# Kernel tuning notes

Hardware: AMD Instinct MI355X
Metric: run time of the kernel (lower is better)

Reference implementation:

```python
import jax, jax.numpy as jnp
import numpy as np

T, B, E, H = 128, 1024, 1024, 1024  # batch must equal hidden (original code uses Whh @ h)


def setup_inputs() -> dict:
    key = jax.random.key(0)
    ks = jax.random.split(key, 10)
    s = 1.0 / np.sqrt(H).astype(np.float32)  # ~xavier scale, avoids gate saturation
    inp = {
        'X': jax.random.normal(ks[0], (T, B, E), dtype=jnp.float32),
        'Wii': jax.random.normal(ks[1], (E, H), dtype=jnp.float32) * s,
        'Whi': jax.random.normal(ks[2], (H, H), dtype=jnp.float32) * s,
        'bi': jnp.zeros((H,), dtype=jnp.float32),
        'Wif': jax.random.normal(ks[3], (E, H), dtype=jnp.float32) * s,
        'Whf': jax.random.normal(ks[4], (H, H), dtype=jnp.float32) * s,
        'bf': jnp.zeros((H,), dtype=jnp.float32),
        'Wig': jax.random.normal(ks[5], (E, H), dtype=jnp.float32) * s,
        'Whg': jax.random.normal(ks[6], (H, H), dtype=jnp.float32) * s,
        'bg': jnp.zeros((H,), dtype=jnp.float32),
        'Wio': jax.random.normal(ks[7], (E, H), dtype=jnp.float32) * s,
        'Who': jax.random.normal(ks[8], (H, H), dtype=jnp.float32) * s,
        'bo': jnp.zeros((H,), dtype=jnp.float32),
    }
    return inp


def reference(X, Wii, Whi, bi, Wif, Whf, bf, Wig, Whg, bg, Wio, Who, bo):
    # Faithful to the original: recurrent term is Whh @ h (NOT h @ Whh),
    # which requires batch == hidden as in the source module.
    batch = X.shape[1]
    hid = Wii.shape[1]
    h0 = jnp.zeros((batch, hid), dtype=X.dtype)
    c0 = jnp.zeros((batch, hid), dtype=X.dtype)

    def step(carry, x_t):
        h, c = carry
        i = jax.nn.sigmoid(x_t @ Wii + Whi @ h + bi)
        f = jax.nn.sigmoid(x_t @ Wif + Whf @ h + bf)
        g = jnp.tanh(x_t @ Wig + Whg @ h + bg)
        o = jax.nn.sigmoid(x_t @ Wio + Who @ h + bo)
        c_new = f * c + i * g
        h_new = o * jnp.tanh(c_new)
        return (h_new, c_new), h_new

    (h_t, c_t), hidden_sequence = jax.lax.scan(step, (h0, c0), X)
    return hidden_sequence, (h_t, c_t)
```

## Files before the change

### kernel.cpp

```cpp
#include <hip/hip_runtime.h>
#include <cstdint>

typedef __attribute__((ext_vector_type(8))) short bf16x8;
typedef __attribute__((ext_vector_type(4))) float f32x4;
typedef __attribute__((ext_vector_type(4))) unsigned int u32x4;

#define AS1 __attribute__((address_space(1)))
#define AS3 __attribute__((address_space(3)))

__device__ __forceinline__ unsigned short f2bf(float f) {
  unsigned int u = __builtin_bit_cast(unsigned int, f);
  return (unsigned short)((u + 0x7fffu + ((u >> 16) & 1u)) >> 16);
}
__device__ __forceinline__ float bf2f(unsigned short h) {
  unsigned int u = ((unsigned int)h) << 16;
  return __builtin_bit_cast(float, u);
}
__device__ __forceinline__ float sigm(float x) { return 1.f / (1.f + __expf(-x)); }
__device__ __forceinline__ float tanh_f(float x) {
  float e = __expf(2.f * x);
  return 1.f - 2.f / (e + 1.f);
}
__device__ __forceinline__ void gload16(const void* g, void* l) {
  __builtin_amdgcn_global_load_lds((const AS1 unsigned int*)g, (AS3 unsigned int*)l, 16, 0, 0);
}
__device__ __forceinline__ int swz(int e) { return e ^ (((e >> 6) & 7) << 3); }


__global__ __launch_bounds__(256) void conv_wh_kernel(
    const float4* __restrict__ w0, const float4* __restrict__ w1,
    const float4* __restrict__ w2, const float4* __restrict__ w3,
    unsigned long long* __restrict__ dst) {
  int i = blockIdx.x * 256 + threadIdx.x;
  int g = i >> 18;
  const float4* s = g == 0 ? w0 : g == 1 ? w1 : g == 2 ? w2 : w3;
  float4 v = s[i & 0x3FFFF];
  unsigned long long p = (unsigned long long)f2bf(v.x) |
                         ((unsigned long long)f2bf(v.y) << 16) |
                         ((unsigned long long)f2bf(v.z) << 32) |
                         ((unsigned long long)f2bf(v.w) << 48);
  dst[i] = p;
}

__global__ __launch_bounds__(256) void conv_wiT_kernel(
    const float* __restrict__ w0, const float* __restrict__ w1,
    const float* __restrict__ w2, const float* __restrict__ w3,
    unsigned short* __restrict__ dst) {
  __shared__ unsigned short ls[64][72];
  int bid = blockIdx.x;
  int g = bid >> 8;
  int t2 = bid & 255;
  int tj = t2 & 15, tk = t2 >> 4;
  const float* W = g == 0 ? w0 : g == 1 ? w1 : g == 2 ? w2 : w3;
  int k0 = tk * 64, j0 = tj * 64;
  int ty = threadIdx.x >> 6, tx = threadIdx.x & 63;
#pragma unroll
  for (int r = 0; r < 16; ++r) {
    int k = k0 + ty * 16 + r;
    ls[tx][ty * 16 + r] = f2bf(W[k * 1024 + j0 + tx]);
  }
  __syncthreads();
#pragma unroll
  for (int r = 0; r < 16; ++r) {
    int jl = ty * 16 + r;
    dst[(size_t)(g * 1024 + j0 + jl) * 1024 + k0 + tx] = ls[jl][tx];
  }
}

__global__ __launch_bounds__(256) void conv_bias_kernel(
    const float* __restrict__ b0, const float* __restrict__ b1,
    const float* __restrict__ b2, const float* __restrict__ b3,
    float* __restrict__ dst) {
  int i = blockIdx.x * 256 + threadIdx.x;
  const float* s = (i >> 10) == 0 ? b0 : (i >> 10) == 1 ? b1 : (i >> 10) == 2 ? b2 : b3;
  dst[i] = s[i & 1023];
}

__global__ __launch_bounds__(256) void conv_x_kernel(
    const float4* __restrict__ src, unsigned long long* __restrict__ dst, int n4) {
  int i = blockIdx.x * 256 + threadIdx.x;
  if (i < n4) {
    float4 v = src[i];
    dst[i] = (unsigned long long)f2bf(v.x) |
             ((unsigned long long)f2bf(v.y) << 16) |
             ((unsigned long long)f2bf(v.z) << 32) |
             ((unsigned long long)f2bf(v.w) << 48);
  }
}

__global__ __launch_bounds__(512) void xproj_gemm_kernel(
    const unsigned short* __restrict__ A,
    const unsigned short* __restrict__ Bt,
    unsigned short* __restrict__ C,
    int Mc) {
  __shared__ __align__(16) unsigned short smem[2][2][256 * 64];
  int xcd = blockIdx.x & 7;
  int i5 = blockIdx.x >> 3;
  int bn = xcd * 2 + (i5 & 1);
  int bm = i5 >> 1;
  int m0 = bm * 256, n0 = bn * 256;
  int tid = threadIdx.x, w = tid >> 6, lane = tid & 63;
  int wm = w >> 2, wn = w & 3;
  int l15 = lane & 15, l4 = lane >> 4;

  f32x4 acc[8][4];
#pragma unroll
  for (int i = 0; i < 8; ++i)
#pragma unroll
    for (int j = 0; j < 4; ++j) acc[i][j] = (f32x4)0.f;

  auto stageHalf = [&](int buf, int kt, int X) {
    int kk = kt * 64;
    unsigned short* dst = &smem[buf][X & 1][0];
    const unsigned short* src = (X & 1) ? Bt : A;
    int gbase = (X & 1) ? n0 : m0;
    int r0 = (X >> 1) * 128;
#pragma unroll
    for (int u = 0; u < 2; ++u) {
      int cid = u * 512 + tid;
      int rl = r0 + (cid >> 3), s = cid & 7;
      int sk = kk + ((s ^ (rl & 7)) << 3);
      gload16(&src[(size_t)(gbase + rl) * 1024 + sk],
              &dst[r0 * 64 + (u * 512 + w * 64) * 8]);
    }
  };
  auto rdA = [&](int buf, int lo, bf16x8 (&arr)[4][2]) {
#pragma unroll
    for (int mf = 0; mf < 4; ++mf)
#pragma unroll
      for (int kss = 0; kss < 2; ++kss) {
        int row = lo * 128 + wm * 64 + mf * 16 + l15;
        arr[mf][kss] =
            *(const bf16x8*)&smem[buf][0][swz(row * 64 + kss * 32 + l4 * 8)];
      }
  };
  auto rdB = [&](int buf, int lo, bf16x8 (&arr)[2][2]) {
#pragma unroll
    for (int nf = 0; nf < 2; ++nf)
#pragma unroll
      for (int kss = 0; kss < 2; ++kss) {
        int row = lo * 128 + wn * 32 + nf * 16 + l15;
        arr[nf][kss] =
            *(const bf16x8*)&smem[buf][1][swz(row * 64 + kss * 32 + l4 * 8)];
      }
  };

  bf16x8 af03[4][2], af47[4][2], bfr01[2][2], bfr23[2][2];

  stageHalf(0, 0, 0); stageHalf(0, 0, 1); stageHalf(0, 0, 2); stageHalf(0, 0, 3);

  for (int t = 0; t < 16; ++t) {
    int c = t & 1;
    if (t < 15) asm volatile("s_waitcnt vmcnt(6)" ::: "memory");
    else        asm volatile("s_waitcnt vmcnt(6)" ::: "memory");
    __builtin_amdgcn_sched_barrier(0);
    __builtin_amdgcn_s_barrier();
    __builtin_amdgcn_sched_barrier(0);
    rdA(c, 0, af03);
    if (t + 1 < 16) stageHalf(c ^ 1, t + 1, 0);
    asm volatile("s_waitcnt lgkmcnt(0)" ::: "memory");
    __builtin_amdgcn_sched_barrier(0);
    if (t > 0) {
      __builtin_amdgcn_s_setprio(1);
#pragma unroll
      for (int mf = 0; mf < 4; ++mf)
#pragma unroll
        for (int nf = 0; nf < 2; ++nf)
#pragma unroll
          for (int kss = 0; kss < 2; ++kss)
            acc[4 + mf][2 + nf] = __builtin_amdgcn_mfma_f32_16x16x32_bf16(
                af47[mf][kss], bfr23[nf][kss], acc[4 + mf][2 + nf], 0, 0, 0);
      __builtin_amdgcn_s_setprio(0);
    }
    if (t < 15) asm volatile("s_waitcnt vmcnt(6)" ::: "memory");
    else        asm volatile("s_waitcnt vmcnt(4)" ::: "memory");
    __builtin_amdgcn_sched_barrier(0);
    __builtin_amdgcn_s_barrier();
    __builtin_amdgcn_sched_barrier(0);
    rdB(c, 0, bfr01);
    if (t + 1 < 16) stageHalf(c ^ 1, t + 1, 1);
    asm volatile("s_waitcnt lgkmcnt(0)" ::: "memory");
    __builtin_amdgcn_sched_barrier(0);
    __builtin_amdgcn_s_setprio(1);
#pragma unroll
    for (int mf = 0; mf < 4; ++mf)
#pragma unroll
      for (int nf = 0; nf < 2; ++nf)
#pragma unroll
        for (int kss = 0; kss < 2; ++kss)
          acc[mf][nf] = __builtin_amdgcn_mfma_f32_16x16x32_bf16(
              af03[mf][kss], bfr01[nf][kss], acc[mf][nf], 0, 0, 0);
    __builtin_amdgcn_s_setprio(0);
    if (t < 15) asm volatile("s_waitcnt vmcnt(6)" ::: "memory");
    else        asm volatile("s_waitcnt vmcnt(2)" ::: "memory");
    __builtin_amdgcn_sched_barrier(0);
    __builtin_amdgcn_s_barrier();
    __builtin_amdgcn_sched_barrier(0);
    rdA(c, 1, af47);
    if (t + 1 < 16) stageHalf(c ^ 1, t + 1, 2);
    asm volatile("s_waitcnt lgkmcnt(0)" ::: "memory");
    __builtin_amdgcn_sched_barrier(0);
    __builtin_amdgcn_s_setprio(1);
#pragma unroll
    for (int mf = 0; mf < 4; ++mf)
#pragma unroll
      for (int nf = 0; nf < 2; ++nf)
#pragma unroll
        for (int kss = 0; kss < 2; ++kss)
          acc[4 + mf][nf] = __builtin_amdgcn_mfma_f32_16x16x32_bf16(
              af47[mf][kss], bfr01[nf][kss], acc[4 + mf][nf], 0, 0, 0);
    __builtin_amdgcn_s_setprio(0);
    if (t < 15) asm volatile("s_waitcnt vmcnt(6)" ::: "memory");
    else        asm volatile("s_waitcnt vmcnt(0)" ::: "memory");
    __builtin_amdgcn_sched_barrier(0);
    __builtin_amdgcn_s_barrier();
    __builtin_amdgcn_sched_barrier(0);
    rdB(c, 1, bfr23);
    if (t + 1 < 16) stageHalf(c ^ 1, t + 1, 3);
    asm volatile("s_waitcnt lgkmcnt(0)" ::: "memory");
    __builtin_amdgcn_sched_barrier(0);
    __builtin_amdgcn_s_setprio(1);
#pragma unroll
    for (int mf = 0; mf < 4; ++mf)
#pragma unroll
      for (int nf = 0; nf < 2; ++nf)
#pragma unroll
        for (int kss = 0; kss < 2; ++kss)
          acc[mf][2 + nf] = __builtin_amdgcn_mfma_f32_16x16x32_bf16(
              af03[mf][kss], bfr23[nf][kss], acc[mf][2 + nf], 0, 0, 0);
    __builtin_amdgcn_s_setprio(0);
  }
  {
    __builtin_amdgcn_s_setprio(1);
#pragma unroll
    for (int mf = 0; mf < 4; ++mf)
#pragma unroll
      for (int nf = 0; nf < 2; ++nf)
#pragma unroll
        for (int kss = 0; kss < 2; ++kss)
          acc[4 + mf][2 + nf] = __builtin_amdgcn_mfma_f32_16x16x32_bf16(
              af47[mf][kss], bfr23[nf][kss], acc[4 + mf][2 + nf], 0, 0, 0);
    __builtin_amdgcn_s_setprio(0);
  }

  unsigned short* lsC = &smem[0][0][0];
#pragma unroll
  for (int h = 0; h < 2; ++h) {
    __syncthreads();
#pragma unroll
    for (int mf = 0; mf < 8; ++mf)
#pragma unroll
      for (int f = 0; f < 2; ++f) {
        int nf = h * 2 + f;
        int rowl = (mf < 4 ? wm * 64 + mf * 16 : 128 + wm * 64 + (mf - 4) * 16)
                   + l4 * 4;
        int coll = wn * 32 + f * 16 + l15;
#pragma unroll
        for (int r = 0; r < 4; ++r)
          lsC[(rowl + r) * 136 + coll] = f2bf(acc[mf][nf][r]);
      }
    __syncthreads();
#pragma unroll
    for (int u = 0; u < 8; ++u) {
      int chunk = u * 512 + tid;
      int row = chunk >> 4, c8 = chunk & 15;
      u32x4 v = *(const u32x4*)&lsC[row * 136 + c8 * 8];
      __builtin_nontemporal_store(
          v, (u32x4*)&C[(size_t)(m0 + row) * 4096 + n0 + h * 128 + c8 * 8]);
    }
  }
}

__global__ __launch_bounds__(256) void lstm_step_kernel(
    const unsigned short* __restrict__ Wh,
    const unsigned short* __restrict__ hT,
    const unsigned short* __restrict__ Xp,
    const float* __restrict__ bias,
    float* __restrict__ cst,
    float* __restrict__ out_h,
    float* __restrict__ out_ht,
    float* __restrict__ out_ct,
    unsigned short* __restrict__ hT_next,
    int isLast) {
  __shared__ unsigned short lsA[3][128 * 64];
  __shared__ unsigned short lsB[3][64 * 64];
  int bx = blockIdx.x;
  int xcd = bx & 7, idx = bx >> 3;
  int bb = xcd * 4 + (idx & 3);
  int bj = idx >> 2;
  int b0 = bb * 32, j0 = bj * 64;
  int tid = threadIdx.x, w = tid >> 6, lane = tid & 63;
  int wm = w >> 1, wn = w & 1;
  int l15 = lane & 15, l4 = lane >> 4;
  int bbase = b0 + wm * 16 + l4 * 4;

  float bias_pre[4][2];
  float c_pre[2][4];
  unsigned short xp_pre[4][2][4];
#pragma unroll
  for (int n = 0; n < 2; ++n) {
    int j = j0 + wn * 32 + n * 16 + l15;
#pragma unroll
    for (int g = 0; g < 4; ++g) bias_pre[g][n] = bias[g * 1024 + j];
#pragma unroll
    for (int r = 0; r < 4; ++r) {
      c_pre[n][r] = cst[(size_t)(bbase + r) * 1024 + j];
#pragma unroll
      for (int g = 0; g < 4; ++g)
        xp_pre[g][n][r] = Xp[(size_t)(bbase + r) * 4096 + g * 1024 + j];
    }
  }

  f32x4 acc[4][2];
#pragma unroll
  for (int g = 0; g < 4; ++g)
#pragma unroll
    for (int n = 0; n < 2; ++n) acc[g][n] = (f32x4)0.f;

  auto stage = [&](int buf, int kk) {
#pragma unroll
    for (int ld = 0; ld < 4; ++ld) {
      int cid = ld * 256 + tid;
      int r = cid >> 3, kc = (cid & 7) * 8;
      int sk = kk + (kc ^ ((r & 7) << 3));
      int grow = ((r >> 4) & 3) * 1024 + b0 + (r >> 6) * 16 + (r & 15);
      gload16(&Wh[(size_t)grow * 1024 + sk], &lsA[buf][(ld * 256 + w * 64) * 8]);
    }
#pragma unroll
    for (int u = 0; u < 2; ++u) {
      int cid = u * 256 + tid;
      int r = cid >> 3, kc = (cid & 7) * 8;
      int sk = kk + (kc ^ ((r & 7) << 3));
      gload16(&hT[(size_t)(j0 + r) * 1024 + sk], &lsB[buf][(u * 256 + w * 64) * 8]);
    }
  };
  auto compute = [&](int buf) {
    bf16x8 af[4][2], bfr[2][2];
#pragma unroll
    for (int g = 0; g < 4; ++g)
#pragma unroll
      for (int kss = 0; kss < 2; ++kss) {
        int e = (wm * 64 + g * 16 + l15) * 64 + kss * 32 + l4 * 8;
        af[g][kss] = *(const bf16x8*)&lsA[buf][swz(e)];
      }
#pragma unroll
    for (int n = 0; n < 2; ++n)
#pragma unroll
      for (int kss = 0; kss < 2; ++kss) {
        int e = (wn * 32 + n * 16 + l15) * 64 + kss * 32 + l4 * 8;
        bfr[n][kss] = *(const bf16x8*)&lsB[buf][swz(e)];
      }
    __builtin_amdgcn_s_setprio(1);
#pragma unroll
    for (int g = 0; g < 4; ++g)
#pragma unroll
      for (int n = 0; n < 2; ++n)
#pragma unroll
        for (int kss = 0; kss < 2; ++kss)
          acc[g][n] = __builtin_amdgcn_mfma_f32_16x16x32_bf16(
              af[g][kss], bfr[n][kss], acc[g][n], 0, 0, 0);
    __builtin_amdgcn_s_setprio(0);
  };

  stage(0, 0);
  stage(1, 64);
#pragma unroll
  for (int it = 0; it < 16; ++it) {
    if (it < 15) asm volatile("s_waitcnt vmcnt(6)" ::: "memory");
    else         asm volatile("s_waitcnt vmcnt(0)" ::: "memory");
    __builtin_amdgcn_sched_barrier(0);
    __builtin_amdgcn_s_barrier();
    __builtin_amdgcn_sched_barrier(0);
    if (it + 2 < 16) stage((it + 2) % 3, (it + 2) * 64);
    compute(it % 3);
    asm volatile("s_waitcnt lgkmcnt(0)" ::: "memory");
    __builtin_amdgcn_sched_barrier(0);
  }

#pragma unroll
  for (int n = 0; n < 2; ++n) {
    int j = j0 + wn * 32 + n * 16 + l15;
    float hn[4], cn[4];
#pragma unroll
    for (int r = 0; r < 4; ++r) {
      int b = bbase + r;
      float pi = acc[0][n][r] + bf2f(xp_pre[0][n][r]) + bias_pre[0][n];
      float pf = acc[1][n][r] + bf2f(xp_pre[1][n][r]) + bias_pre[1][n];
      float pg = acc[2][n][r] + bf2f(xp_pre[2][n][r]) + bias_pre[2][n];
      float po = acc[3][n][r] + bf2f(xp_pre[3][n][r]) + bias_pre[3][n];
      float ig = sigm(pi), fg = sigm(pf), gg = tanh_f(pg), og = sigm(po);
      float c_new = fg * c_pre[n][r] + ig * gg;
      cst[(size_t)b * 1024 + j] = c_new;
      cn[r] = c_new;
      hn[r] = og * tanh_f(c_new);
      __builtin_nontemporal_store(hn[r], &out_h[(size_t)b * 1024 + j]);
    }
    unsigned long long hp = (unsigned long long)f2bf(hn[0]) |
                            ((unsigned long long)f2bf(hn[1]) << 16) |
                            ((unsigned long long)f2bf(hn[2]) << 32) |
                            ((unsigned long long)f2bf(hn[3]) << 48);
    *(unsigned long long*)&hT_next[(size_t)j * 1024 + bbase] = hp;
    if (isLast) {
#pragma unroll
      for (int r = 0; r < 4; ++r) {
        int b = bbase + r;
        __builtin_nontemporal_store(hn[r], &out_ht[(size_t)b * 1024 + j]);
        __builtin_nontemporal_store(cn[r], &out_ct[(size_t)b * 1024 + j]);
      }
    }
  }
}

extern "C" void kernel_launch(void* const* d_in, const int* in_sizes, int n_in,
                              void* d_out, int out_size, void* d_ws, size_t ws_size,
                              hipStream_t stream) {
  const float* X   = (const float*)d_in[0];
  const float* Wii = (const float*)d_in[1];
  const float* Whi = (const float*)d_in[2];
  const float* bi  = (const float*)d_in[3];
  const float* Wif = (const float*)d_in[4];
  const float* Whf = (const float*)d_in[5];
  const float* bfv = (const float*)d_in[6];
  const float* Wig = (const float*)d_in[7];
  const float* Whg = (const float*)d_in[8];
  const float* bg  = (const float*)d_in[9];
  const float* Wio = (const float*)d_in[10];
  const float* Who = (const float*)d_in[11];
  const float* bo  = (const float*)d_in[12];
  float* out = (float*)d_out;

  char* wsp = (char*)d_ws;
  size_t off = 0;
  auto walloc = [&](size_t b) -> void* {
    void* p = wsp + off;
    off += (b + 255) & ~(size_t)255;
    return p;
  };
  unsigned short* WiT = (unsigned short*)walloc(4096ull * 1024 * 2);
  unsigned short* Wh  = (unsigned short*)walloc(4096ull * 1024 * 2);
  float* bias = (float*)walloc(4096 * 4);
  unsigned short* hT0 = (unsigned short*)walloc(1024ull * 1024 * 2);
  unsigned short* hT1 = (unsigned short*)walloc(1024ull * 1024 * 2);
  float* cbuf = (float*)walloc(1024ull * 1024 * 4);
  size_t fixed = off;

  long long avail = (long long)ws_size - (long long)fixed - (1ll << 20);
  int Tc = (int)(avail / (10ll << 20));
  if (Tc < 1) Tc = 1;
  if (Tc > 128) Tc = 128;
  unsigned short* Xbf = (unsigned short*)walloc((size_t)Tc * 1024 * 1024 * 2);
  unsigned short* Xp  = (unsigned short*)walloc((size_t)Tc * 1024 * 4096 * 2);

  conv_wh_kernel<<<4096, 256, 0, stream>>>((const float4*)Whi, (const float4*)Whf,
                                           (const float4*)Whg, (const float4*)Who,
                                           (unsigned long long*)Wh);
  conv_wiT_kernel<<<1024, 256, 0, stream>>>(Wii, Wif, Wig, Wio, WiT);
  conv_bias_kernel<<<16, 256, 0, stream>>>(bi, bfv, bg, bo, bias);
  hipMemsetAsync(hT0, 0, 1024ull * 1024 * 2, stream);
  hipMemsetAsync(cbuf, 0, 1024ull * 1024 * 4, stream);

  for (int t0 = 0; t0 < 128; t0 += Tc) {
    int tc = (128 - t0 < Tc) ? (128 - t0) : Tc;
    int n4 = tc * 262144;
    conv_x_kernel<<<n4 / 256, 256, 0, stream>>>(
        (const float4*)(X + (size_t)t0 * 1048576),
        (unsigned long long*)Xbf, n4);
    xproj_gemm_kernel<<<tc * 64, 512, 0, stream>>>(Xbf, WiT, Xp, tc * 1024);
    for (int i = 0; i < tc; ++i) {
      int t = t0 + i;
      lstm_step_kernel<<<512, 256, 0, stream>>>(
          Wh, (t & 1) ? hT1 : hT0,
          Xp + (size_t)i * 1024 * 4096,
          bias, cbuf,
          out + (size_t)t * 1048576,
          out + 134217728ull,
          out + 135266304ull,
          (t & 1) ? hT0 : hT1,
          (t == 127) ? 1 : 0);
    }
  }
}
```

Before: 3.362 ms.

## Restructure GEMM main loop into two-phase schedule with fewer barriers

Reorganizes the double-buffered MFMA main loop from four barrier-separated sub-phases into two, each issuing two stage loads and two LDS fragment reads while deferring cluster computations across phase boundaries (cl2/cl3 of previous step run at start of next). This halves the number of workgroup barriers and explicit lgkmcnt waits per K-tile, aiming to overlap LDS reads and global loads with MFMA work. It relies on correct vmcnt accounting and on register fragments staying live across iterations, which increases register pressure and the risk of LDS hazards.

New measurement: 3.702 ms. 10.1% more time.

```diff
diff --git a/kernel.cpp b/kernel.cpp
--- a/kernel.cpp
+++ b/kernel.cpp
@@ -147,101 +147,80 @@
 
   bf16x8 af03[4][2], af47[4][2], bfr01[2][2], bfr23[2][2];
 
+  auto cl1 = [&] {
+#pragma unroll
+    for (int mf = 0; mf < 4; ++mf)
+#pragma unroll
+      for (int nf = 0; nf < 2; ++nf)
+#pragma unroll
+        for (int k = 0; k < 2; ++k)
+          acc[mf][nf] = __builtin_amdgcn_mfma_f32_16x16x32_bf16(
+              af03[mf][k], bfr01[nf][k], acc[mf][nf], 0, 0, 0);
+  };
+  auto cl2 = [&] {
+#pragma unroll
+    for (int mf = 0; mf < 4; ++mf)
+#pragma unroll
+      for (int nf = 0; nf < 2; ++nf)
+#pragma unroll
+        for (int k = 0; k < 2; ++k)
+          acc[4 + mf][nf] = __builtin_amdgcn_mfma_f32_16x16x32_bf16(
+              af47[mf][k], bfr01[nf][k], acc[4 + mf][nf], 0, 0, 0);
+  };
+  auto cl3 = [&] {
+#pragma unroll
+    for (int mf = 0; mf < 4; ++mf)
+#pragma unroll
+      for (int nf = 0; nf < 2; ++nf)
+#pragma unroll
+        for (int k = 0; k < 2; ++k)
+          acc[mf][2 + nf] = __builtin_amdgcn_mfma_f32_16x16x32_bf16(
+              af03[mf][k], bfr23[nf][k], acc[mf][2 + nf], 0, 0, 0);
+  };
+  auto cl4 = [&] {
+#pragma unroll
+    for (int mf = 0; mf < 4; ++mf)
+#pragma unroll
+      for (int nf = 0; nf < 2; ++nf)
+#pragma unroll
+        for (int k = 0; k < 2; ++k)
+          acc[4 + mf][2 + nf] = __builtin_amdgcn_mfma_f32_16x16x32_bf16(
+              af47[mf][k], bfr23[nf][k], acc[4 + mf][2 + nf], 0, 0, 0);
+  };
+
   stageHalf(0, 0, 0); stageHalf(0, 0, 1); stageHalf(0, 0, 2); stageHalf(0, 0, 3);
 
   for (int t = 0; t < 16; ++t) {
     int c = t & 1;
-    if (t < 15) asm volatile("s_waitcnt vmcnt(6)" ::: "memory");
-    else        asm volatile("s_waitcnt vmcnt(6)" ::: "memory");
+    asm volatile("s_waitcnt vmcnt(4)" ::: "memory");
     __builtin_amdgcn_sched_barrier(0);
     __builtin_amdgcn_s_barrier();
-    __builtin_amdgcn_sched_barrier(0);
-    rdA(c, 0, af03);
-    if (t + 1 < 16) stageHalf(c ^ 1, t + 1, 0);
-    asm volatile("s_waitcnt lgkmcnt(0)" ::: "memory");
     __builtin_amdgcn_sched_barrier(0);
     if (t > 0) {
       __builtin_amdgcn_s_setprio(1);
-#pragma unroll
-      for (int mf = 0; mf < 4; ++mf)
-#pragma unroll
-        for (int nf = 0; nf < 2; ++nf)
-#pragma unroll
-          for (int kss = 0; kss < 2; ++kss)
-            acc[4 + mf][2 + nf] = __builtin_amdgcn_mfma_f32_16x16x32_bf16(
-                af47[mf][kss], bfr23[nf][kss], acc[4 + mf][2 + nf], 0, 0, 0);
+      cl2();
+      cl3();
       __builtin_amdgcn_s_setprio(0);
     }
-    if (t < 15) asm volatile("s_waitcnt vmcnt(6)" ::: "memory");
-    else        asm volatile("s_waitcnt vmcnt(4)" ::: "memory");
+    rdA(c, 0, af03);
+    rdB(c, 0, bfr01);
+    if (t + 1 < 16) { stageHalf(c ^ 1, t + 1, 0); stageHalf(c ^ 1, t + 1, 1); }
+    if (t < 15) asm volatile("s_waitcnt vmcnt(4)" ::: "memory");
+    else        asm volatile("s_waitcnt vmcnt(0)" ::: "memory");
     __builtin_amdgcn_sched_barrier(0);
     __builtin_amdgcn_s_barrier();
     __builtin_amdgcn_sched_barrier(0);
-    rdB(c, 0, bfr01);
-    if (t + 1 < 16) stageHalf(c ^ 1, t + 1, 1);
-    asm volatile("s_waitcnt lgkmcnt(0)" ::: "memory");
-    __builtin_amdgcn_sched_barrier(0);
     __builtin_amdgcn_s_setprio(1);
-#pragma unroll
-    for (int mf = 0; mf < 4; ++mf)
-#pragma unroll
-      for (int nf = 0; nf < 2; ++nf)
-#pragma unroll
-        for (int kss = 0; kss < 2; ++kss)
-          acc[mf][nf] = __builtin_amdgcn_mfma_f32_16x16x32_bf16(
-              af03[mf][kss], bfr01[nf][kss], acc[mf][nf], 0, 0, 0);
+    cl1();
+    if (t > 0) cl4();
     __builtin_amdgcn_s_setprio(0);
-    if (t < 15) asm volatile("s_waitcnt vmcnt(6)" ::: "memory");
-    else        asm volatile("s_waitcnt vmcnt(2)" ::: "memory");
-    __builtin_amdgcn_sched_barrier(0);
-    __builtin_amdgcn_s_barrier();
-    __builtin_amdgcn_sched_barrier(0);
     rdA(c, 1, af47);
-    if (t + 1 < 16) stageHalf(c ^ 1, t + 1, 2);
-    asm volatile("s_waitcnt lgkmcnt(0)" ::: "memory");
-    __builtin_amdgcn_sched_barrier(0);
-    __builtin_amdgcn_s_setprio(1);
-#pragma unroll
-    for (int mf = 0; mf < 4; ++mf)
-#pragma unroll
-      for (int nf = 0; nf < 2; ++nf)
-#pragma unroll
-        for (int kss = 0; kss < 2; ++kss)
-          acc[4 + mf][nf] = __builtin_amdgcn_mfma_f32_16x16x32_bf16(
-              af47[mf][kss], bfr01[nf][kss], acc[4 + mf][nf], 0, 0, 0);
-    __builtin_amdgcn_s_setprio(0);
-    if (t < 15) asm volatile("s_waitcnt vmcnt(6)" ::: "memory");
-    else        asm volatile("s_waitcnt vmcnt(0)" ::: "memory");
-    __builtin_amdgcn_sched_barrier(0);
-    __builtin_amdgcn_s_barrier();
-    __builtin_amdgcn_sched_barrier(0);
     rdB(c, 1, bfr23);
-    if (t + 1 < 16) stageHalf(c ^ 1, t + 1, 3);
-    asm volatile("s_waitcnt lgkmcnt(0)" ::: "memory");
-    __builtin_amdgcn_sched_barrier(0);
-    __builtin_amdgcn_s_setprio(1);
-#pragma unroll
-    for (int mf = 0; mf < 4; ++mf)
-#pragma unroll
-      for (int nf = 0; nf < 2; ++nf)
-#pragma unroll
-        for (int kss = 0; kss < 2; ++kss)
-          acc[mf][2 + nf] = __builtin_amdgcn_mfma_f32_16x16x32_bf16(
-              af03[mf][kss], bfr23[nf][kss], acc[mf][2 + nf], 0, 0, 0);
-    __builtin_amdgcn_s_setprio(0);
-  }
-  {
-    __builtin_amdgcn_s_setprio(1);
-#pragma unroll
-    for (int mf = 0; mf < 4; ++mf)
-#pragma unroll
-      for (int nf = 0; nf < 2; ++nf)
-#pragma unroll
-        for (int kss = 0; kss < 2; ++kss)
-          acc[4 + mf][2 + nf] = __builtin_amdgcn_mfma_f32_16x16x32_bf16(
-              af47[mf][kss], bfr23[nf][kss], acc[4 + mf][2 + nf], 0, 0, 0);
-    __builtin_amdgcn_s_setprio(0);
-  }
+    if (t + 1 < 16) { stageHalf(c ^ 1, t + 1, 2); stageHalf(c ^ 1, t + 1, 3); }
+  }
+  __builtin_amdgcn_s_setprio(1);
+  cl2(); cl3(); cl4();
+  __builtin_amdgcn_s_setprio(0);
 
   unsigned short* lsC = &smem[0][0][0];
 #pragma unroll
```
